# Optimization experiments

Measured on AMD Instinct MI355X. Metric: run time of the kernel, lower is better.

The kernel has to match this reference:

```python
import jax, jax.numpy as jnp
import numpy as np

# Module hyperparameters (from init_kwargs)
K = 1.0                       # init_curvature (registered buffer, non-trainable)
HOPFIELD_DIM = 64
BETA = 1.0 / np.sqrt(float(HOPFIELD_DIM))  # beta=None default -> 1/sqrt(d_h)
EPS = 1e-7

# ---- Lorentz / hyperboloid ops (geoopt conventions, curvature param k>0) ----

def _to_tangent0(x):
    # x: (..., d) Euclidean -> (..., d+1) in T_0 H via [0, x], norm-clipped to 3.5
    zeros = jnp.zeros(x.shape[:-1] + (1,), x.dtype)
    x = jnp.concatenate([zeros, x], axis=-1)
    n = jnp.linalg.norm(x, axis=-1, keepdims=True)
    factor = jnp.minimum(3.5 / (n + 1e-7), 1.0)
    return x * factor

def expmap0(x_euc):
    # (..., d) Euclidean -> (..., d+1) on hyperboloid via Exp_0([0, x])
    u = _to_tangent0(x_euc)
    x = u[..., 1:]
    sqrtk = jnp.sqrt(K)
    xn = jnp.maximum(jnp.linalg.norm(x, axis=-1, keepdims=True), EPS)
    theta = xn / sqrtk
    return jnp.concatenate(
        [sqrtk * jnp.cosh(theta), sqrtk * jnp.sinh(theta) * x / xn], axis=-1)

def logmap0(y):
    # (..., d+1) on hyperboloid -> (..., d) tangent at origin (spatial part)
    sqrtk = jnp.sqrt(K)
    y0 = y[..., :1]
    yr = y[..., 1:]
    yn = jnp.maximum(jnp.linalg.norm(yr, axis=-1, keepdims=True), EPS)
    d = sqrtk * jnp.arccosh(jnp.maximum(y0 / sqrtk, 1.0 + EPS))
    return d * yr / yn

def minkowski_inner(u, v):
    # <u,v>_L = -u0 v0 + sum_i u_i v_i ; returns (...) without last dim
    return -u[..., 0] * v[..., 0] + jnp.sum(u[..., 1:] * v[..., 1:], axis=-1)

# ---- KFCore forward ----

def _kfcore(queries, keys, values, Wq, bq, Wk, bk, Wv, bv):
    sqrtk = jnp.sqrt(K)
    Qe = queries @ Wq.T + bq                     # (B,S,d_h)
    Ke = keys @ Wk.T + bk                        # (B,M,d_h)
    Ve = (values @ Wk.T + bk) @ Wv.T + bv        # (B,M,d_out)
    Q = expmap0(Qe)                              # (B,S,d+1)
    Kh = expmap0(Ke)                             # (B,M,d+1)
    V = expmap0(Ve)                              # (B,M,d+1)

    dp1 = Q.shape[-1]
    sign = jnp.concatenate([-jnp.ones((1,), Q.dtype), jnp.ones((dp1 - 1,), Q.dtype)])

    # Minkowski inner pairwise: (B,S,M)
    sims = jnp.einsum('bsd,bmd->bsm', Q * sign, Kh)
    alpha = jax.nn.softmax(-BETA * sims, axis=-1)          # (B,S,M)

    # Karcher flow: tangent_mean = sum_m alpha * logmap_Q(V_m)
    # logmap_x(y) = dist(x,y) * (y + (<x,y>/k) x) / ||y + (<x,y>/k) x||_L
    ip = jnp.einsum('bsd,bmd->bsm', Q * sign, V)           # <Q_s, V_m>_L
    dist = sqrtk * jnp.arccosh(jnp.maximum(-ip / K, 1.0 + EPS))
    qq = minkowski_inner(Q, Q)[:, :, None]                 # (B,S,1)
    vv = minkowski_inner(V, V)[:, None, :]                 # (B,1,M)
    c = ip / K
    nomin_sq = vv + 2.0 * c * ip + c * c * qq              # ||nomin||_L^2, (B,S,M)
    denom = jnp.sqrt(jnp.maximum(nomin_sq, EPS))
    w = alpha * dist / denom                               # (B,S,M)
    # sum_m w * (V_m + c * Q_s)  -- avoids the (B,S,M,d+1) logmap tensor
    tm = jnp.einsum('bsm,bmd->bsd', w, V) \
         + jnp.sum(w * c, axis=-1, keepdims=True) * Q      # (B,S,d+1)

    # expmap_Q(tm) = cosh(||tm||/sqrtk) Q + sqrtk sinh(||tm||/sqrtk) tm/||tm||
    un = jnp.sqrt(jnp.maximum(minkowski_inner(tm, tm), EPS))[..., None]
    th = un / sqrtk
    z = jnp.cosh(th) * Q + sqrtk * jnp.sinh(th) * tm / un
    return logmap0(z)                                      # (B,S,d_out)


def setup_inputs() -> dict:
    key = jax.random.key(0)
    ks = jax.random.split(key, 9)
    B, S, M = 2, 2048, 4096
    SD, MD, DH, DO = 256, 256, 64, 64
    sq = 1.0 / np.sqrt(SD)
    sm = 1.0 / np.sqrt(MD)
    sh = 1.0 / np.sqrt(DH)
    return {
        'queries': jax.random.normal(ks[0], (B, S, SD), jnp.float32),
        'keys':    jax.random.normal(ks[1], (B, M, MD), jnp.float32),
        'values':  jax.random.normal(ks[2], (B, M, MD), jnp.float32),
        'Wq': jax.random.normal(ks[3], (DH, SD), jnp.float32) * sq,
        'bq': jax.random.normal(ks[4], (DH,), jnp.float32) * sq,
        'Wk': jax.random.normal(ks[5], (DH, MD), jnp.float32) * sm,
        'bk': jax.random.normal(ks[6], (DH,), jnp.float32) * sm,
        'Wv': jax.random.normal(ks[7], (DO, DH), jnp.float32) * sh,
        'bv': jax.random.normal(ks[8], (DO,), jnp.float32) * sh,
    }


def reference(queries, keys, values, Wq, bq, Wk, bk, Wv, bv):
    return _kfcore(queries, keys, values, Wq, bq, Wk, bk, Wv, bv)
```

## Files before the change

kernel.cpp:

```cpp
#include <hip/hip_runtime.h>
#include <math.h>

#define BETA  0.125f
#define SHIFT 30.0f
#define EPSF  1e-7f

typedef __attribute__((ext_vector_type(8))) short short8;
typedef __attribute__((ext_vector_type(4))) short short4v;
typedef __attribute__((ext_vector_type(4))) float f32x4;

__device__ __forceinline__ unsigned short bf16_rne(float x) {
  unsigned int u = __float_as_uint(x);
  return (unsigned short)((u + 0x7fffu + ((u >> 16) & 1u)) >> 16);
}
__device__ __forceinline__ float bf16_tof(unsigned short h) {
  return __uint_as_float(((unsigned int)h) << 16);
}
__device__ __forceinline__ void split2(float x, unsigned short& h, unsigned short& l) {
  unsigned int u = __float_as_uint(x);
  unsigned int hr = (u + 0x7fffu + ((u >> 16) & 1u)) & 0xffff0000u;
  h = (unsigned short)(hr >> 16);
  l = bf16_rne(x - __uint_as_float(hr));
}

#define ZERO_F4 68608

__global__ __launch_bounds__(256) void proj_kernel(
    const float* __restrict__ Xq, const float* __restrict__ Xk,
    const float* __restrict__ Xv,
    const float* __restrict__ Wq, const float* __restrict__ bq,
    const float* __restrict__ Wk, const float* __restrict__ bk,
    const float* __restrict__ Wv, const float* __restrict__ bv,
    float* __restrict__ Q0, float* __restrict__ K0, float* __restrict__ V0,
    unsigned short* __restrict__ Qh, unsigned short* __restrict__ Ql,
    unsigned short* __restrict__ Kh, unsigned short* __restrict__ Kl,
    unsigned short* __restrict__ Vh, unsigned short* __restrict__ Vl,
    unsigned short* __restrict__ Vth, unsigned short* __restrict__ Vtl,
    float* __restrict__ zeroRegion)
{
  __shared__ float Xs[32 * 64];
  __shared__ float Ws[64 * 64];
  __shared__ unsigned int Tr[32 * 65];

  const int bid = blockIdx.x;
  const int tid = threadIdx.x;

  {
    int idx = bid * 256 + tid;
    if (idx < ZERO_F4)
      *(float4*)&zeroRegion[idx * 4] = make_float4(0.f, 0.f, 0.f, 0.f);
  }

  const float *X, *W, *bias;
  float* y0;
  unsigned short *yh, *yl;
  bool dbl;
  int rowBase;
  if (bid < 256)      { X = Xv; W = Wk; bias = bk; y0 = V0; yh = Vh; yl = Vl; rowBase = bid << 5;         dbl = true;  }
  else if (bid < 512) { X = Xk; W = Wk; bias = bk; y0 = K0; yh = Kh; yl = Kl; rowBase = (bid - 256) << 5; dbl = false; }
  else                { X = Xq; W = Wq; bias = bq; y0 = Q0; yh = Qh; yl = Ql; rowBase = (bid - 512) << 5; dbl = false; }

  const int ty = tid >> 4, tx = tid & 15;
  const int ty2 = ty << 1, tx4 = tx << 2;
  const int tyq = ty >> 1;

  float acc[2][4];
#pragma unroll
  for (int j = 0; j < 4; ++j) {
    float bj = bias[tx4 + j];
#pragma unroll
    for (int i = 0; i < 2; ++i) acc[i][j] = bj;
  }

  for (int kc = 0; kc < 4; ++kc) {
#pragma unroll
    for (int q = 0; q < 2; ++q) {
      int f = tid + (q << 8);
      int r = f >> 4, g = f & 15;
      int sw = (r << 6) + ((g ^ (r >> 2)) << 2);
      *(float4*)&Xs[sw] = *(const float4*)&X[(rowBase + r) * 256 + (kc << 6) + (g << 2)];
    }
#pragma unroll
    for (int q = 0; q < 4; ++q) {
      int f = tid + (q << 8);
      int r = f >> 4, g = f & 15;
      int sw = (r << 6) + ((g ^ (r >> 2)) << 2);
      *(float4*)&Ws[sw] = *(const float4*)&W[r * 256 + (kc << 6) + (g << 2)];
    }
    __syncthreads();
#pragma unroll 4
    for (int kk = 0; kk < 64; kk += 4) {
      const int gk = kk >> 2;
      float4 xa[2], wb[4];
#pragma unroll
      for (int i = 0; i < 2; ++i)
        xa[i] = *(const float4*)&Xs[((ty2 + i) << 6) + ((gk ^ tyq) << 2)];
#pragma unroll
      for (int j = 0; j < 4; ++j)
        wb[j] = *(const float4*)&Ws[((tx4 + j) << 6) + ((gk ^ tx) << 2)];
#pragma unroll
      for (int i = 0; i < 2; ++i)
#pragma unroll
        for (int j = 0; j < 4; ++j)
          acc[i][j] += xa[i].x * wb[j].x + xa[i].y * wb[j].y +
                       xa[i].z * wb[j].z + xa[i].w * wb[j].w;
    }
    __syncthreads();
  }

  if (dbl) {
#pragma unroll
    for (int i = 0; i < 2; ++i) {
      float4 v = make_float4(acc[i][0], acc[i][1], acc[i][2], acc[i][3]);
      *(float4*)&Xs[((ty2 + i) << 6) + ((tx ^ tyq) << 2)] = v;
    }
#pragma unroll
    for (int q = 0; q < 4; ++q) {
      int f = tid + (q << 8);
      int r = f >> 4, g = f & 15;
      int sw = (r << 6) + ((g ^ (r >> 2)) << 2);
      *(float4*)&Ws[sw] = *(const float4*)&Wv[(r << 6) + (g << 2)];
    }
#pragma unroll
    for (int j = 0; j < 4; ++j) {
      float bj = bv[tx4 + j];
#pragma unroll
      for (int i = 0; i < 2; ++i) acc[i][j] = bj;
    }
    __syncthreads();
#pragma unroll 4
    for (int kk = 0; kk < 64; kk += 4) {
      const int gk = kk >> 2;
      float4 xa[2], wb[4];
#pragma unroll
      for (int i = 0; i < 2; ++i)
        xa[i] = *(const float4*)&Xs[((ty2 + i) << 6) + ((gk ^ tyq) << 2)];
#pragma unroll
      for (int j = 0; j < 4; ++j)
        wb[j] = *(const float4*)&Ws[((tx4 + j) << 6) + ((gk ^ tx) << 2)];
#pragma unroll
      for (int i = 0; i < 2; ++i)
#pragma unroll
        for (int j = 0; j < 4; ++j)
          acc[i][j] += xa[i].x * wb[j].x + xa[i].y * wb[j].y +
                       xa[i].z * wb[j].z + xa[i].w * wb[j].w;
    }
  }

  float n2p[2];
#pragma unroll
  for (int i = 0; i < 2; ++i)
    n2p[i] = acc[i][0] * acc[i][0] + acc[i][1] * acc[i][1] +
             acc[i][2] * acc[i][2] + acc[i][3] * acc[i][3];
#pragma unroll
  for (int i = 0; i < 2; ++i) {
    n2p[i] += __shfl_xor(n2p[i], 1);
    n2p[i] += __shfl_xor(n2p[i], 2);
    n2p[i] += __shfl_xor(n2p[i], 4);
    n2p[i] += __shfl_xor(n2p[i], 8);
  }
  unsigned short hv[2][4], lv[2][4];
#pragma unroll
  for (int i = 0; i < 2; ++i) {
    float n = sqrtf(n2p[i]);
    float factor = fminf(3.5f / (n + EPSF), 1.0f);
    float xn = fmaxf(n * factor, EPSF);
    float et = __expf(xn);
    float rt = __builtin_amdgcn_rcpf(et);
    float ch = 0.5f * (et + rt);
    float sh = 0.5f * (et - rt);
    float scale = sh * factor * __builtin_amdgcn_rcpf(xn);
    int row = rowBase + ty2 + i;
    if (tx == 0) y0[row] = ch;
#pragma unroll
    for (int j = 0; j < 4; ++j) split2(acc[i][j] * scale, hv[i][j], lv[i][j]);
    unsigned int* ph = (unsigned int*)(yh + row * 64 + tx4);
    ph[0] = (unsigned int)hv[i][0] | ((unsigned int)hv[i][1] << 16);
    ph[1] = (unsigned int)hv[i][2] | ((unsigned int)hv[i][3] << 16);
    unsigned int* pl = (unsigned int*)(yl + row * 64 + tx4);
    pl[0] = (unsigned int)lv[i][0] | ((unsigned int)lv[i][1] << 16);
    pl[1] = (unsigned int)lv[i][2] | ((unsigned int)lv[i][3] << 16);
  }

  if (dbl) {
#pragma unroll
    for (int i = 0; i < 2; ++i)
#pragma unroll
      for (int j = 0; j < 4; ++j)
        Tr[(ty2 + i) * 65 + tx4 + j] = (unsigned int)hv[i][j];
    __syncthreads();
    {
      int d = tid >> 2;
      int seg = (tid & 3) << 3;
      unsigned int o[4];
#pragma unroll
      for (int k = 0; k < 4; ++k)
        o[k] = Tr[(seg + 2 * k) * 65 + d] | (Tr[(seg + 2 * k + 1) * 65 + d] << 16);
      *(uint4*)&Vth[d * 8192 + rowBase + seg] = make_uint4(o[0], o[1], o[2], o[3]);
    }
    __syncthreads();
#pragma unroll
    for (int i = 0; i < 2; ++i)
#pragma unroll
      for (int j = 0; j < 4; ++j)
        Tr[(ty2 + i) * 65 + tx4 + j] = (unsigned int)lv[i][j];
    __syncthreads();
    {
      int d = tid >> 2;
      int seg = (tid & 3) << 3;
      unsigned int o[4];
#pragma unroll
      for (int k = 0; k < 4; ++k)
        o[k] = Tr[(seg + 2 * k) * 65 + d] | (Tr[(seg + 2 * k + 1) * 65 + d] << 16);
      *(uint4*)&Vtl[d * 8192 + rowBase + seg] = make_uint4(o[0], o[1], o[2], o[3]);
    }
  }
}

__global__ void __attribute__((amdgpu_waves_per_eu(2, 2)))
__launch_bounds__(256) attn_kernel(
    const float* __restrict__ Q0g, const unsigned short* __restrict__ Qh,
    const unsigned short* __restrict__ Ql,
    const float* __restrict__ K0g, const unsigned short* __restrict__ Khg,
    const unsigned short* __restrict__ Klg,
    const float* __restrict__ V0g, const unsigned short* __restrict__ Vhg,
    const unsigned short* __restrict__ Vlg,
    const unsigned short* __restrict__ Vthg, const unsigned short* __restrict__ Vtlg,
    float* __restrict__ Tacc, float* __restrict__ T0acc,
    float* __restrict__ Lacc, float* __restrict__ WCacc)
{
  __shared__ unsigned short LB[6 * 4608];

  const int tid = threadIdx.x;
  const int wave = tid >> 6, lane = tid & 63;
  const int lm = lane & 15;
  const int lg = lane >> 4;
  const int bid = blockIdx.x;
  const int slice = bid & 15;
  const int t = bid >> 4;
  const int b = t >> 4;
  const int sT = t & 15;
  const int sBase = b * 2048 + sT * 128 + wave * 32;

  unsigned short* wbase = LB + wave * 2176;

  short8 qf[2][2][2];
#pragma unroll
  for (int si = 0; si < 2; ++si)
#pragma unroll
    for (int ks = 0; ks < 2; ++ks) {
      int idx = (sBase + si * 16 + lm) * 64 + ks * 32 + lg * 8;
      qf[si][ks][0] = *(const short8*)(Qh + idx);
      qf[si][ks][1] = *(const short8*)(Ql + idx);
    }
  float q0r[2][4];
#pragma unroll
  for (int si = 0; si < 2; ++si)
#pragma unroll
    for (int r = 0; r < 4; ++r)
      q0r[si][r] = Q0g[sBase + si * 16 + lg * 4 + r];

  f32x4 accT[2][4];
  float Lp[2][4], WCp[2][4], T0p[2][4];
#pragma unroll
  for (int si = 0; si < 2; ++si)
#pragma unroll
    for (int r = 0; r < 4; ++r) {
      Lp[si][r] = 0.f; WCp[si][r] = 0.f; T0p[si][r] = 0.f;
    }
#pragma unroll
  for (int si = 0; si < 2; ++si)
#pragma unroll
    for (int dj = 0; dj < 4; ++dj) accT[si][dj] = f32x4{0.f, 0.f, 0.f, 0.f};

  const int mSliceBase = b * 4096 + slice * 256;
  const int frow = tid >> 3;
  const int fc8 = (tid & 7) << 3;
  for (int mc = 0; mc < 4; ++mc) {
    const int mCh = mSliceBase + (mc << 6);

#pragma unroll
    for (int q = 0; q < 2; ++q) {
      int row = frow + (q << 5);
      int goff = (mCh + row) * 64 + fc8;
      int loff = row * 72 + fc8;
      *(uint4*)&LB[loff]            = *(const uint4*)&Khg[goff];
      *(uint4*)&LB[4608 + loff]     = *(const uint4*)&Klg[goff];
      *(uint4*)&LB[2 * 4608 + loff] = *(const uint4*)&Vhg[goff];
      *(uint4*)&LB[3 * 4608 + loff] = *(const uint4*)&Vlg[goff];
      int gofft = row * 8192 + mCh + fc8;
      *(uint4*)&LB[4 * 4608 + loff] = *(const uint4*)&Vthg[gofft];
      *(uint4*)&LB[5 * 4608 + loff] = *(const uint4*)&Vtlg[gofft];
    }
    float k0r[4], v0r[4];
#pragma unroll
    for (int mj = 0; mj < 4; ++mj) {
      k0r[mj] = K0g[mCh + mj * 16 + lm];
      v0r[mj] = V0g[mCh + mj * 16 + lm];
    }
    __syncthreads();

    f32x4 sims[2][4], ipv[2][4];
#pragma unroll
    for (int si = 0; si < 2; ++si)
#pragma unroll
      for (int mj = 0; mj < 4; ++mj) {
        sims[si][mj] = f32x4{0.f, 0.f, 0.f, 0.f};
        ipv[si][mj]  = f32x4{0.f, 0.f, 0.f, 0.f};
      }
#pragma unroll
    for (int mj = 0; mj < 4; ++mj) {
#pragma unroll
      for (int ks = 0; ks < 2; ++ks) {
        int off = (mj * 16 + lm) * 72 + ks * 32 + lg * 8;
        short8 kh = *(const short8*)&LB[off];
        short8 kl = *(const short8*)&LB[4608 + off];
        short8 vh = *(const short8*)&LB[2 * 4608 + off];
        short8 vl = *(const short8*)&LB[3 * 4608 + off];
#pragma unroll
        for (int si = 0; si < 2; ++si) {
          sims[si][mj] = __builtin_amdgcn_mfma_f32_16x16x32_bf16(qf[si][ks][0], kh, sims[si][mj], 0, 0, 0);
          sims[si][mj] = __builtin_amdgcn_mfma_f32_16x16x32_bf16(qf[si][ks][0], kl, sims[si][mj], 0, 0, 0);
          sims[si][mj] = __builtin_amdgcn_mfma_f32_16x16x32_bf16(qf[si][ks][1], kh, sims[si][mj], 0, 0, 0);
          ipv[si][mj]  = __builtin_amdgcn_mfma_f32_16x16x32_bf16(qf[si][ks][0], vh, ipv[si][mj], 0, 0, 0);
          ipv[si][mj]  = __builtin_amdgcn_mfma_f32_16x16x32_bf16(qf[si][ks][0], vl, ipv[si][mj], 0, 0, 0);
          ipv[si][mj]  = __builtin_amdgcn_mfma_f32_16x16x32_bf16(qf[si][ks][1], vh, ipv[si][mj], 0, 0, 0);
        }
      }
    }
    __syncthreads();

#pragma unroll
    for (int si = 0; si < 2; ++si)
#pragma unroll
      for (int mj = 0; mj < 4; ++mj)
#pragma unroll
        for (int r = 0; r < 4; ++r) {
          float c  = ipv[si][mj][r]  - q0r[si][r] * v0r[mj];
          float sm = sims[si][mj][r] - q0r[si][r] * k0r[mj];
          float x = -c;
          float s2 = fmaxf(fmaf(x, x, -1.0f), EPSF);
          float rs = __builtin_amdgcn_rsqf(s2);
          float dist = __logf(fmaf(s2, rs, x));
          float e = __expf(fmaf(-BETA, sm, -SHIFT));
          float w = e * dist * rs;
          unsigned short wu = bf16_rne(w);
          float wb = bf16_tof(wu);
          Lp[si][r]  += e;
          WCp[si][r] += wb * c;
          T0p[si][r] += wb * v0r[mj];
          wbase[(si * 16 + lg * 4 + r) * 68 + mj * 16 + lm] = wu;
        }

#pragma unroll
    for (int ks = 0; ks < 2; ++ks) {
      short8 wa[2];
#pragma unroll
      for (int si = 0; si < 2; ++si) {
        const unsigned short* p = wbase + (si * 16 + lm) * 68 + ks * 32 + lg * 8;
        short4v a0 = *(const short4v*)p;
        short4v a1 = *(const short4v*)(p + 4);
        wa[si] = __builtin_shufflevector(a0, a1, 0, 1, 2, 3, 4, 5, 6, 7);
      }
#pragma unroll
      for (int dj = 0; dj < 4; ++dj) {
        int off = (dj * 16 + lm) * 72 + ks * 32 + lg * 8;
        short8 th = *(const short8*)&LB[4 * 4608 + off];
        short8 tl = *(const short8*)&LB[5 * 4608 + off];
#pragma unroll
        for (int si = 0; si < 2; ++si) {
          accT[si][dj] = __builtin_amdgcn_mfma_f32_16x16x32_bf16(wa[si], th, accT[si][dj], 0, 0, 0);
          accT[si][dj] = __builtin_amdgcn_mfma_f32_16x16x32_bf16(wa[si], tl, accT[si][dj], 0, 0, 0);
        }
      }
    }
    __syncthreads();
  }

#pragma unroll
  for (int si = 0; si < 2; ++si)
#pragma unroll
    for (int r = 0; r < 4; ++r)
#pragma unroll
      for (int off = 1; off < 16; off <<= 1) {
        Lp[si][r]  += __shfl_xor(Lp[si][r], off);
        WCp[si][r] += __shfl_xor(WCp[si][r], off);
        T0p[si][r] += __shfl_xor(T0p[si][r], off);
      }

#pragma unroll
  for (int si = 0; si < 2; ++si)
#pragma unroll
    for (int r = 0; r < 4; ++r) {
      int row = sBase + si * 16 + lg * 4 + r;
#pragma unroll
      for (int dj = 0; dj < 4; ++dj)
        unsafeAtomicAdd(&Tacc[row * 64 + dj * 16 + lm], accT[si][dj][r]);
      if (lm == 0) {
        unsafeAtomicAdd(&Lacc[row],  Lp[si][r]);
        unsafeAtomicAdd(&WCacc[row], WCp[si][r]);
        unsafeAtomicAdd(&T0acc[row], T0p[si][r]);
      }
    }
}

__global__ __launch_bounds__(256) void combine_kernel(
    const float* __restrict__ Q0, const unsigned short* __restrict__ Qh,
    const unsigned short* __restrict__ Ql,
    const float* __restrict__ Tacc, const float* __restrict__ T0acc,
    const float* __restrict__ Lacc, const float* __restrict__ WCacc,
    float* __restrict__ out)
{
  int wid = (blockIdx.x << 2) + (threadIdx.x >> 6);
  int lane = threadIdx.x & 63;

  int qi = wid * 64 + lane;
  float Tsum = Tacc[qi];
  float T0 = T0acc[wid];
  float L  = Lacc[wid];
  float WC = WCacc[wid];

  float qd = bf16_tof(Qh[qi]) + bf16_tof(Ql[qi]);
  float q0 = Q0[wid];
  float invL = 1.0f / L;
  float td = Tsum * invL;
  float t0 = T0 * invL;
  float wc = WC * invL;

  double tt = (double)td * (double)td;
#pragma unroll
  for (int off = 1; off < 64; off <<= 1) tt += __shfl_xor(tt, off);
  tt -= (double)t0 * (double)t0;
  double mk = tt + (double)wc * (double)wc;

  float un = (float)sqrt(fmax(mk, 1e-12));
  float eu = __expf(un);
  float ru = 1.0f / eu;
  float ch = 0.5f * (eu + ru);
  float shu = 0.5f * (eu - ru) / un;

  float tmd = td + wc * qd;
  float tm0 = t0 + wc * q0;
  float zd = ch * qd + shu * tmd;
  float z0 = ch * q0 + shu * tm0;

  float p2 = zd * zd;
#pragma unroll
  for (int off = 1; off < 64; off <<= 1) p2 += __shfl_xor(p2, off);
  float yn = fmaxf(sqrtf(p2), EPSF);
  float zc = fmaxf(z0, 1.0f + EPSF);
  float dl = __logf(zc + sqrtf(fmaxf(zc * zc - 1.0f, 0.f)));
  out[qi] = dl * zd / yn;
}

extern "C" void kernel_launch(void* const* d_in, const int* in_sizes, int n_in,
                              void* d_out, int out_size, void* d_ws, size_t ws_size,
                              hipStream_t stream)
{
  const float* queries = (const float*)d_in[0];
  const float* keys    = (const float*)d_in[1];
  const float* values  = (const float*)d_in[2];
  const float* Wq      = (const float*)d_in[3];
  const float* bq      = (const float*)d_in[4];
  const float* Wk      = (const float*)d_in[5];
  const float* bk      = (const float*)d_in[6];
  const float* Wv      = (const float*)d_in[7];
  const float* bv      = (const float*)d_in[8];
  float* out = (float*)d_out;
  float* ws  = (float*)d_ws;

  float* Q0 = ws;
  float* K0 = ws + 4096;
  float* V0 = ws + 12288;
  unsigned short* Qh  = (unsigned short*)(ws + 20480);
  unsigned short* Ql  = (unsigned short*)(ws + 151552);
  unsigned short* Kh  = (unsigned short*)(ws + 282624);
  unsigned short* Kl  = (unsigned short*)(ws + 544768);
  unsigned short* Vh  = (unsigned short*)(ws + 806912);
  unsigned short* Vl  = (unsigned short*)(ws + 1069056);
  unsigned short* Vth = (unsigned short*)(ws + 1331200);
  unsigned short* Vtl = (unsigned short*)(ws + 1593344);
  float* Tacc  = ws + 1855488;
  float* T0acc = ws + 2117632;
  float* Lacc  = ws + 2121728;
  float* WCacc = ws + 2125824;

  proj_kernel<<<640, 256, 0, stream>>>(queries, keys, values, Wq, bq, Wk, bk,
                                       Wv, bv, Q0, K0, V0, Qh, Ql, Kh, Kl,
                                       Vh, Vl, Vth, Vtl, Tacc);
  attn_kernel<<<512, 256, 0, stream>>>(
      Q0, Qh, Ql, K0, Kh, Kl, V0, Vh, Vl, Vth, Vtl,
      Tacc, T0acc, Lacc, WCacc);
  combine_kernel<<<1024, 256, 0, stream>>>(
      Q0, Qh, Ql, Tacc, T0acc, Lacc, WCacc, out);
}
```

Measured before the change: 157.5 us.

## Fuse projection, attention and combine into one persistent kernel with grid barriers

Merges the three kernels into a single 512-block persistent kernel. Blocks 0–127 each take a second projection tile, and software grid barriers built on an atomic counter separate the projection, attention and combine phases. This removes two kernel launches and their gaps. In exchange it adds a memset launch, requires all 512 blocks to be co-resident (enforced via waves_per_eu), and leaves the projection phase load-imbalanced.

```diff
diff --git a/kernel.cpp b/kernel.cpp
--- a/kernel.cpp
+++ b/kernel.cpp
@@ -25,7 +25,20 @@
 
 #define ZERO_F4 68608
 
-__global__ __launch_bounds__(256) void proj_kernel(
+__device__ __forceinline__ void gbar(unsigned int* cnt, unsigned int target) {
+  __syncthreads();
+  if (threadIdx.x == 0) {
+    __threadfence();
+    atomicAdd(cnt, 1u);
+    while (__hip_atomic_load(cnt, __ATOMIC_RELAXED, __HIP_MEMORY_SCOPE_AGENT) < target)
+      __builtin_amdgcn_s_sleep(8);
+  }
+  __syncthreads();
+  __threadfence();
+}
+
+__global__ void __attribute__((amdgpu_waves_per_eu(2, 2)))
+__launch_bounds__(256) fused_kernel(
     const float* __restrict__ Xq, const float* __restrict__ Xk,
     const float* __restrict__ Xv,
     const float* __restrict__ Wq, const float* __restrict__ bq,
@@ -36,421 +49,420 @@
     unsigned short* __restrict__ Kh, unsigned short* __restrict__ Kl,
     unsigned short* __restrict__ Vh, unsigned short* __restrict__ Vl,
     unsigned short* __restrict__ Vth, unsigned short* __restrict__ Vtl,
-    float* __restrict__ zeroRegion)
+    float* __restrict__ Tacc, float* __restrict__ T0acc,
+    float* __restrict__ Lacc, float* __restrict__ WCacc,
+    unsigned int* __restrict__ bar, float* __restrict__ out)
 {
-  __shared__ float Xs[32 * 64];
-  __shared__ float Ws[64 * 64];
-  __shared__ unsigned int Tr[32 * 65];
+  __shared__ unsigned short LB[6 * 4608];
 
   const int bid = blockIdx.x;
   const int tid = threadIdx.x;
 
   {
-    int idx = bid * 256 + tid;
-    if (idx < ZERO_F4)
-      *(float4*)&zeroRegion[idx * 4] = make_float4(0.f, 0.f, 0.f, 0.f);
-  }
-
-  const float *X, *W, *bias;
-  float* y0;
-  unsigned short *yh, *yl;
-  bool dbl;
-  int rowBase;
-  if (bid < 256)      { X = Xv; W = Wk; bias = bk; y0 = V0; yh = Vh; yl = Vl; rowBase = bid << 5;         dbl = true;  }
-  else if (bid < 512) { X = Xk; W = Wk; bias = bk; y0 = K0; yh = Kh; yl = Kl; rowBase = (bid - 256) << 5; dbl = false; }
-  else                { X = Xq; W = Wq; bias = bq; y0 = Q0; yh = Qh; yl = Ql; rowBase = (bid - 512) << 5; dbl = false; }
-
-  const int ty = tid >> 4, tx = tid & 15;
-  const int ty2 = ty << 1, tx4 = tx << 2;
-  const int tyq = ty >> 1;
-
-  float acc[2][4];
-#pragma unroll
-  for (int j = 0; j < 4; ++j) {
-    float bj = bias[tx4 + j];
-#pragma unroll
-    for (int i = 0; i < 2; ++i) acc[i][j] = bj;
-  }
-
-  for (int kc = 0; kc < 4; ++kc) {
-#pragma unroll
-    for (int q = 0; q < 2; ++q) {
-      int f = tid + (q << 8);
-      int r = f >> 4, g = f & 15;
-      int sw = (r << 6) + ((g ^ (r >> 2)) << 2);
-      *(float4*)&Xs[sw] = *(const float4*)&X[(rowBase + r) * 256 + (kc << 6) + (g << 2)];
+    float* Xs = (float*)(void*)LB;
+    float* Ws = (float*)(void*)(LB + 4096);
+    unsigned int* Tr = (unsigned int*)(void*)(LB + 12288);
+
+    {
+      int idx = bid * 256 + tid;
+      if (idx < ZERO_F4)
+        *(float4*)&Tacc[idx * 4] = make_float4(0.f, 0.f, 0.f, 0.f);
     }
-#pragma unroll
-    for (int q = 0; q < 4; ++q) {
-      int f = tid + (q << 8);
-      int r = f >> 4, g = f & 15;
-      int sw = (r << 6) + ((g ^ (r >> 2)) << 2);
-      *(float4*)&Ws[sw] = *(const float4*)&W[r * 256 + (kc << 6) + (g << 2)];
-    }
-    __syncthreads();
+
+    const int ty = tid >> 4, tx = tid & 15;
+    const int ty2 = ty << 1, tx4 = tx << 2;
+    const int tyq = ty >> 1;
+
+    for (int pass = 0; pass < 2; ++pass) {
+      if (pass == 1 && bid >= 128) break;
+      const int t = bid + pass * 512;
+
+      const float *X, *W, *bias;
+      float* y0;
+      unsigned short *yh, *yl;
+      bool dbl;
+      int rowBase;
+      if (t < 256)      { X = Xv; W = Wk; bias = bk; y0 = V0; yh = Vh; yl = Vl; rowBase = t << 5;         dbl = true;  }
+      else if (t < 512) { X = Xk; W = Wk; bias = bk; y0 = K0; yh = Kh; yl = Kl; rowBase = (t - 256) << 5; dbl = false; }
+      else              { X = Xq; W = Wq; bias = bq; y0 = Q0; yh = Qh; yl = Ql; rowBase = (t - 512) << 5; dbl = false; }
+
+      __syncthreads();
+
+      float acc[2][4];
+#pragma unroll
+      for (int j = 0; j < 4; ++j) {
+        float bj = bias[tx4 + j];
+#pragma unroll
+        for (int i = 0; i < 2; ++i) acc[i][j] = bj;
+      }
+
+      for (int kc = 0; kc < 4; ++kc) {
+#pragma unroll
+        for (int q = 0; q < 2; ++q) {
+          int f = tid + (q << 8);
+          int r = f >> 4, g = f & 15;
+          int sw = (r << 6) + ((g ^ (r >> 2)) << 2);
+          *(float4*)&Xs[sw] = *(const float4*)&X[(rowBase + r) * 256 + (kc << 6) + (g << 2)];
+        }
+#pragma unroll
+        for (int q = 0; q < 4; ++q) {
+          int f = tid + (q << 8);
+          int r = f >> 4, g = f & 15;
+          int sw = (r << 6) + ((g ^ (r >> 2)) << 2);
+          *(float4*)&Ws[sw] = *(const float4*)&W[r * 256 + (kc << 6) + (g << 2)];
+        }
+        __syncthreads();
 #pragma unroll 4
-    for (int kk = 0; kk < 64; kk += 4) {
-      const int gk = kk >> 2;
-      float4 xa[2], wb[4];
+        for (int kk = 0; kk < 64; kk += 4) {
+          const int gk = kk >> 2;
+          float4 xa[2], wb[4];
+#pragma unroll
+          for (int i = 0; i < 2; ++i)
+            xa[i] = *(const float4*)&Xs[((ty2 + i) << 6) + ((gk ^ tyq) << 2)];
+#pragma unroll
+          for (int j = 0; j < 4; ++j)
+            wb[j] = *(const float4*)&Ws[((tx4 + j) << 6) + ((gk ^ tx) << 2)];
+#pragma unroll
+          for (int i = 0; i < 2; ++i)
+#pragma unroll
+            for (int j = 0; j < 4; ++j)
+              acc[i][j] += xa[i].x * wb[j].x + xa[i].y * wb[j].y +
+                           xa[i].z * wb[j].z + xa[i].w * wb[j].w;
+        }
+        __syncthreads();
+      }
+
+      if (dbl) {
+#pragma unroll
+        for (int i = 0; i < 2; ++i) {
+          float4 v = make_float4(acc[i][0], acc[i][1], acc[i][2], acc[i][3]);
+          *(float4*)&Xs[((ty2 + i) << 6) + ((tx ^ tyq) << 2)] = v;
+        }
+#pragma unroll
+        for (int q = 0; q < 4; ++q) {
+          int f = tid + (q << 8);
+          int r = f >> 4, g = f & 15;
+          int sw = (r << 6) + ((g ^ (r >> 2)) << 2);
+          *(float4*)&Ws[sw] = *(const float4*)&Wv[(r << 6) + (g << 2)];
+        }
+#pragma unroll
+        for (int j = 0; j < 4; ++j) {
+          float bj = bv[tx4 + j];
+#pragma unroll
+          for (int i = 0; i < 2; ++i) acc[i][j] = bj;
+        }
+        __syncthreads();
+#pragma unroll 4
+        for (int kk = 0; kk < 64; kk += 4) {
+          const int gk = kk >> 2;
+          float4 xa[2], wb[4];
+#pragma unroll
+          for (int i = 0; i < 2; ++i)
+            xa[i] = *(const float4*)&Xs[((ty2 + i) << 6) + ((gk ^ tyq) << 2)];
+#pragma unroll
+          for (int j = 0; j < 4; ++j)
+            wb[j] = *(const float4*)&Ws[((tx4 + j) << 6) + ((gk ^ tx) << 2)];
+#pragma unroll
+          for (int i = 0; i < 2; ++i)
+#pragma unroll
+            for (int j = 0; j < 4; ++j)
+              acc[i][j] += xa[i].x * wb[j].x + xa[i].y * wb[j].y +
+                           xa[i].z * wb[j].z + xa[i].w * wb[j].w;
+        }
+      }
+
+      float n2p[2];
 #pragma unroll
       for (int i = 0; i < 2; ++i)
-        xa[i] = *(const float4*)&Xs[((ty2 + i) << 6) + ((gk ^ tyq) << 2)];
-#pragma unroll
-      for (int j = 0; j < 4; ++j)
-        wb[j] = *(const float4*)&Ws[((tx4 + j) << 6) + ((gk ^ tx) << 2)];
-#pragma unroll
-      for (int i = 0; i < 2; ++i)
-#pragma unroll
-        for (int j = 0; j < 4; ++j)
-          acc[i][j] += xa[i].x * wb[j].x + xa[i].y * wb[j].y +
-                       xa[i].z * wb[j].z + xa[i].w * wb[j].w;
-    }
-    __syncthreads();
-  }
-
-  if (dbl) {
-#pragma unroll
-    for (int i = 0; i < 2; ++i) {
-      float4 v = make_float4(acc[i][0], acc[i][1], acc[i][2], acc[i][3]);
-      *(float4*)&Xs[((ty2 + i) << 6) + ((tx ^ tyq) << 2)] = v;
-    }
-#pragma unroll
-    for (int q = 0; q < 4; ++q) {
-      int f = tid + (q << 8);
-      int r = f >> 4, g = f & 15;
-      int sw = (r << 6) + ((g ^ (r >> 2)) << 2);
-      *(float4*)&Ws[sw] = *(const float4*)&Wv[(r << 6) + (g << 2)];
-    }
-#pragma unroll
-    for (int j = 0; j < 4; ++j) {
-      float bj = bv[tx4 + j];
-#pragma unroll
-      for (int i = 0; i < 2; ++i) acc[i][j] = bj;
-    }
-    __syncthreads();
-#pragma unroll 4
-    for (int kk = 0; kk < 64; kk += 4) {
-      const int gk = kk >> 2;
-      float4 xa[2], wb[4];
-#pragma unroll
-      for (int i = 0; i < 2; ++i)
-        xa[i] = *(const float4*)&Xs[((ty2 + i) << 6) + ((gk ^ tyq) << 2)];
-#pragma unroll
-      for (int j = 0; j < 4; ++j)
-        wb[j] = *(const float4*)&Ws[((tx4 + j) << 6) + ((gk ^ tx) << 2)];
-#pragma unroll
-      for (int i = 0; i < 2; ++i)
-#pragma unroll
-        for (int j = 0; j < 4; ++j)
-          acc[i][j] += xa[i].x * wb[j].x + xa[i].y * wb[j].y +
-                       xa[i].z * wb[j].z + xa[i].w * wb[j].w;
+        n2p[i] = acc[i][0] * acc[i][0] + acc[i][1] * acc[i][1] +
+                 acc[i][2] * acc[i][2] + acc[i][3] * acc[i][3];
+#pragma unroll
+      for (int i = 0; i < 2; ++i) {
+        n2p[i] += __shfl_xor(n2p[i], 1);
+        n2p[i] += __shfl_xor(n2p[i], 2);
+        n2p[i] += __shfl_xor(n2p[i], 4);
+        n2p[i] += __shfl_xor(n2p[i], 8);
+      }
+      unsigned short hv[2][4], lv[2][4];
+#pragma unroll
+      for (int i = 0; i < 2; ++i) {
+        float n = sqrtf(n2p[i]);
+        float factor = fminf(3.5f / (n + EPSF), 1.0f);
+        float xn = fmaxf(n * factor, EPSF);
+        float et = __expf(xn);
+        float rt = __builtin_amdgcn_rcpf(et);
+        float ch = 0.5f * (et + rt);
+        float sh = 0.5f * (et - rt);
+        float scale = sh * factor * __builtin_amdgcn_rcpf(xn);
+        int row = rowBase + ty2 + i;
+        if (tx == 0) y0[row] = ch;
+#pragma unroll
+        for (int j = 0; j < 4; ++j) split2(acc[i][j] * scale, hv[i][j], lv[i][j]);
+        unsigned int* ph = (unsigned int*)(yh + row * 64 + tx4);
+        ph[0] = (unsigned int)hv[i][0] | ((unsigned int)hv[i][1] << 16);
+        ph[1] = (unsigned int)hv[i][2] | ((unsigned int)hv[i][3] << 16);
+        unsigned int* pl = (unsigned int*)(yl + row * 64 + tx4);
+        pl[0] = (unsigned int)lv[i][0] | ((unsigned int)lv[i][1] << 16);
+        pl[1] = (unsigned int)lv[i][2] | ((unsigned int)lv[i][3] << 16);
+      }
+
+      if (dbl) {
+#pragma unroll
+        for (int i = 0; i < 2; ++i)
+#pragma unroll
+          for (int j = 0; j < 4; ++j)
+            Tr[(ty2 + i) * 65 + tx4 + j] = (unsigned int)hv[i][j];
+        __syncthreads();
+        {
+          int d = tid >> 2;
+          int seg = (tid & 3) << 3;
+          unsigned int o[4];
+#pragma unroll
+          for (int k = 0; k < 4; ++k)
+            o[k] = Tr[(seg + 2 * k) * 65 + d] | (Tr[(seg + 2 * k + 1) * 65 + d] << 16);
+          *(uint4*)&Vth[d * 8192 + rowBase + seg] = make_uint4(o[0], o[1], o[2], o[3]);
+        }
+        __syncthreads();
+#pragma unroll
+        for (int i = 0; i < 2; ++i)
+#pragma unroll
+          for (int j = 0; j < 4; ++j)
+            Tr[(ty2 + i) * 65 + tx4 + j] = (unsigned int)lv[i][j];
+        __syncthreads();
+        {
+          int d = tid >> 2;
+          int seg = (tid & 3) << 3;
+          unsigned int o[4];
+#pragma unroll
+          for (int k = 0; k < 4; ++k)
+            o[k] = Tr[(seg + 2 * k) * 65 + d] | (Tr[(seg + 2 * k + 1) * 65 + d] << 16);
+          *(uint4*)&Vtl[d * 8192 + rowBase + seg] = make_uint4(o[0], o[1], o[2], o[3]);
+        }
+      }
     }
   }
 
-  float n2p[2];
-#pragma unroll
-  for (int i = 0; i < 2; ++i)
-    n2p[i] = acc[i][0] * acc[i][0] + acc[i][1] * acc[i][1] +
-             acc[i][2] * acc[i][2] + acc[i][3] * acc[i][3];
-#pragma unroll
-  for (int i = 0; i < 2; ++i) {
-    n2p[i] += __shfl_xor(n2p[i], 1);
-    n2p[i] += __shfl_xor(n2p[i], 2);
-    n2p[i] += __shfl_xor(n2p[i], 4);
-    n2p[i] += __shfl_xor(n2p[i], 8);
+  gbar(bar, 512u);
+
+  {
+    const int wave = tid >> 6, lane = tid & 63;
+    const int lm = lane & 15;
+    const int lg = lane >> 4;
+    const int slice = bid & 15;
+    const int t = bid >> 4;
+    const int b = t >> 4;
+    const int sT = t & 15;
+    const int sBase = b * 2048 + sT * 128 + wave * 32;
+
+    unsigned short* wbase = LB + wave * 2176;
+
+    short8 qf[2][2][2];
+#pragma unroll
+    for (int si = 0; si < 2; ++si)
+#pragma unroll
+      for (int ks = 0; ks < 2; ++ks) {
+        int idx = (sBase + si * 16 + lm) * 64 + ks * 32 + lg * 8;
+        qf[si][ks][0] = *(const short8*)(Qh + idx);
+        qf[si][ks][1] = *(const short8*)(Ql + idx);
+      }
+    float q0r[2][4];
+#pragma unroll
+    for (int si = 0; si < 2; ++si)
+#pragma unroll
+      for (int r = 0; r < 4; ++r)
+        q0r[si][r] = Q0[sBase + si * 16 + lg * 4 + r];
+
+    f32x4 accT[2][4];
+    float Lp[2][4], WCp[2][4], T0p[2][4];
+#pragma unroll
+    for (int si = 0; si < 2; ++si)
+#pragma unroll
+      for (int r = 0; r < 4; ++r) {
+        Lp[si][r] = 0.f; WCp[si][r] = 0.f; T0p[si][r] = 0.f;
+      }
+#pragma unroll
+    for (int si = 0; si < 2; ++si)
+#pragma unroll
+      for (int dj = 0; dj < 4; ++dj) accT[si][dj] = f32x4{0.f, 0.f, 0.f, 0.f};
+
+    const int mSliceBase = b * 4096 + slice * 256;
+    const int frow = tid >> 3;
+    const int fc8 = (tid & 7) << 3;
+    for (int mc = 0; mc < 4; ++mc) {
+      const int mCh = mSliceBase + (mc << 6);
+
+#pragma unroll
+      for (int q = 0; q < 2; ++q) {
+        int row = frow + (q << 5);
+        int goff = (mCh + row) * 64 + fc8;
+        int loff = row * 72 + fc8;
+        *(uint4*)&LB[loff]            = *(const uint4*)&Kh[goff];
+        *(uint4*)&LB[4608 + loff]     = *(const uint4*)&Kl[goff];
+        *(uint4*)&LB[2 * 4608 + loff] = *(const uint4*)&Vh[goff];
+        *(uint4*)&LB[3 * 4608 + loff] = *(const uint4*)&Vl[goff];
+        int gofft = row * 8192 + mCh + fc8;
+        *(uint4*)&LB[4 * 4608 + loff] = *(const uint4*)&Vth[gofft];
+        *(uint4*)&LB[5 * 4608 + loff] = *(const uint4*)&Vtl[gofft];
+      }
+      float k0r[4], v0r[4];
+#pragma unroll
+      for (int mj = 0; mj < 4; ++mj) {
+        k0r[mj] = K0[mCh + mj * 16 + lm];
+        v0r[mj] = V0[mCh + mj * 16 + lm];
+      }
+      __syncthreads();
+
+      f32x4 sims[2][4], ipv[2][4];
+#pragma unroll
+      for (int si = 0; si < 2; ++si)
+#pragma unroll
+        for (int mj = 0; mj < 4; ++mj) {
+          sims[si][mj] = f32x4{0.f, 0.f, 0.f, 0.f};
+          ipv[si][mj]  = f32x4{0.f, 0.f, 0.f, 0.f};
+        }
+#pragma unroll
+      for (int mj = 0; mj < 4; ++mj) {
+#pragma unroll
+        for (int ks = 0; ks < 2; ++ks) {
+          int off = (mj * 16 + lm) * 72 + ks * 32 + lg * 8;
+          short8 kh = *(const short8*)&LB[off];
+          short8 kl = *(const short8*)&LB[4608 + off];
+          short8 vh = *(const short8*)&LB[2 * 4608 + off];
+          short8 vl = *(const short8*)&LB[3 * 4608 + off];
+#pragma unroll
+          for (int si = 0; si < 2; ++si) {
+            sims[si][mj] = __builtin_amdgcn_mfma_f32_16x16x32_bf16(qf[si][ks][0], kh, sims[si][mj], 0, 0, 0);
+            sims[si][mj] = __builtin_amdgcn_mfma_f32_16x16x32_bf16(qf[si][ks][0], kl, sims[si][mj], 0, 0, 0);
+            sims[si][mj] = __builtin_amdgcn_mfma_f32_16x16x32_bf16(qf[si][ks][1], kh, sims[si][mj], 0, 0, 0);
+            ipv[si][mj]  = __builtin_amdgcn_mfma_f32_16x16x32_bf16(qf[si][ks][0], vh, ipv[si][mj], 0, 0, 0);
+            ipv[si][mj]  = __builtin_amdgcn_mfma_f32_16x16x32_bf16(qf[si][ks][0], vl, ipv[si][mj], 0, 0, 0);
+            ipv[si][mj]  = __builtin_amdgcn_mfma_f32_16x16x32_bf16(qf[si][ks][1], vh, ipv[si][mj], 0, 0, 0);
+          }
+        }
+      }
+      __syncthreads();
+
+#pragma unroll
+      for (int si = 0; si < 2; ++si)
+#pragma unroll
+        for (int mj = 0; mj < 4; ++mj)
+#pragma unroll
+          for (int r = 0; r < 4; ++r) {
+            float c  = ipv[si][mj][r]  - q0r[si][r] * v0r[mj];
+            float sm = sims[si][mj][r] - q0r[si][r] * k0r[mj];
+            float x = -c;
+            float s2 = fmaxf(fmaf(x, x, -1.0f), EPSF);
+            float rs = __builtin_amdgcn_rsqf(s2);
+            float dist = __logf(fmaf(s2, rs, x));
+            float e = __expf(fmaf(-BETA, sm, -SHIFT));
+            float w = e * dist * rs;
+            unsigned short wu = bf16_rne(w);
+            float wb = bf16_tof(wu);
+            Lp[si][r]  += e;
+            WCp[si][r] += wb * c;
+            T0p[si][r] += wb * v0r[mj];
+            wbase[(si * 16 + lg * 4 + r) * 68 + mj * 16 + lm] = wu;
+          }
+
+#pragma unroll
+      for (int ks = 0; ks < 2; ++ks) {
+        short8 wa[2];
+#pragma unroll
+        for (int si = 0; si < 2; ++si) {
+          const unsigned short* p = wbase + (si * 16 + lm) * 68 + ks * 32 + lg * 8;
+          short4v a0 = *(const short4v*)p;
+          short4v a1 = *(const short4v*)(p + 4);
+          wa[si] = __builtin_shufflevector(a0, a1, 0, 1, 2, 3, 4, 5, 6, 7);
+        }
+#pragma unroll
+        for (int dj = 0; dj < 4; ++dj) {
+          int off = (dj * 16 + lm) * 72 + ks * 32 + lg * 8;
+          short8 th = *(const short8*)&LB[4 * 4608 + off];
+          short8 tl = *(const short8*)&LB[5 * 4608 + off];
+#pragma unroll
+          for (int si = 0; si < 2; ++si) {
+            accT[si][dj] = __builtin_amdgcn_mfma_f32_16x16x32_bf16(wa[si], th, accT[si][dj], 0, 0, 0);
+            accT[si][dj] = __builtin_amdgcn_mfma_f32_16x16x32_bf16(wa[si], tl, accT[si][dj], 0, 0, 0);
+          }
+        }
+      }
+      __syncthreads();
+    }
+
+#pragma unroll
+    for (int si = 0; si < 2; ++si)
+#pragma unroll
+      for (int r = 0; r < 4; ++r)
+#pragma unroll
+        for (int off = 1; off < 16; off <<= 1) {
+          Lp[si][r]  += __shfl_xor(Lp[si][r], off);
+          WCp[si][r] += __shfl_xor(WCp[si][r], off);
+          T0p[si][r] += __shfl_xor(T0p[si][r], off);
+        }
+
+#pragma unroll
+    for (int si = 0; si < 2; ++si)
+#pragma unroll
+      for (int r = 0; r < 4; ++r) {
+        int row = sBase + si * 16 + lg * 4 + r;
+#pragma unroll
+        for (int dj = 0; dj < 4; ++dj)
+          unsafeAtomicAdd(&Tacc[row * 64 + dj * 16 + lm], accT[si][dj][r]);
+        if (lm == 0) {
+          unsafeAtomicAdd(&Lacc[row],  Lp[si][r]);
+          unsafeAtomicAdd(&WCacc[row], WCp[si][r]);
+          unsafeAtomicAdd(&T0acc[row], T0p[si][r]);
+        }
+      }
   }
-  unsigned short hv[2][4], lv[2][4];
-#pragma unroll
-  for (int i = 0; i < 2; ++i) {
-    float n = sqrtf(n2p[i]);
-    float factor = fminf(3.5f / (n + EPSF), 1.0f);
-    float xn = fmaxf(n * factor, EPSF);
-    float et = __expf(xn);
-    float rt = __builtin_amdgcn_rcpf(et);
-    float ch = 0.5f * (et + rt);
-    float sh = 0.5f * (et - rt);
-    float scale = sh * factor * __builtin_amdgcn_rcpf(xn);
-    int row = rowBase + ty2 + i;
-    if (tx == 0) y0[row] = ch;
-#pragma unroll
-    for (int j = 0; j < 4; ++j) split2(acc[i][j] * scale, hv[i][j], lv[i][j]);
-    unsigned int* ph = (unsigned int*)(yh + row * 64 + tx4);
-    ph[0] = (unsigned int)hv[i][0] | ((unsigned int)hv[i][1] << 16);
-    ph[1] = (unsigned int)hv[i][2] | ((unsigned int)hv[i][3] << 16);
-    unsigned int* pl = (unsigned int*)(yl + row * 64 + tx4);
-    pl[0] = (unsigned int)lv[i][0] | ((unsigned int)lv[i][1] << 16);
-    pl[1] = (unsigned int)lv[i][2] | ((unsigned int)lv[i][3] << 16);
-  }
-
-  if (dbl) {
-#pragma unroll
-    for (int i = 0; i < 2; ++i)
-#pragma unroll
-      for (int j = 0; j < 4; ++j)
-        Tr[(ty2 + i) * 65 + tx4 + j] = (unsigned int)hv[i][j];
-    __syncthreads();
-    {
-      int d = tid >> 2;
-      int seg = (tid & 3) << 3;
-      unsigned int o[4];
-#pragma unroll
-      for (int k = 0; k < 4; ++k)
-        o[k] = Tr[(seg + 2 * k) * 65 + d] | (Tr[(seg + 2 * k + 1) * 65 + d] << 16);
-      *(uint4*)&Vth[d * 8192 + rowBase + seg] = make_uint4(o[0], o[1], o[2], o[3]);
-    }
-    __syncthreads();
-#pragma unroll
-    for (int i = 0; i < 2; ++i)
-#pragma unroll
-      for (int j = 0; j < 4; ++j)
-        Tr[(ty2 + i) * 65 + tx4 + j] = (unsigned int)lv[i][j];
-    __syncthreads();
-    {
-      int d = tid >> 2;
-      int seg = (tid & 3) << 3;
-      unsigned int o[4];
-#pragma unroll
-      for (int k = 0; k < 4; ++k)
-        o[k] = Tr[(seg + 2 * k) * 65 + d] | (Tr[(seg + 2 * k + 1) * 65 + d] << 16);
-      *(uint4*)&Vtl[d * 8192 + rowBase + seg] = make_uint4(o[0], o[1], o[2], o[3]);
+
+  gbar(bar + 1, 512u);
+
+  {
+    const int wave = tid >> 6, lane = tid & 63;
+    const int wid0 = bid * 4 + wave;
+#pragma unroll
+    for (int half = 0; half < 2; ++half) {
+      int wid = wid0 + half * 2048;
+      int qi = wid * 64 + lane;
+      float Tsum = Tacc[qi];
+      float T0 = T0acc[wid];
+      float L  = Lacc[wid];
+      float WC = WCacc[wid];
+
+      float qd = bf16_tof(Qh[qi]) + bf16_tof(Ql[qi]);
+      float q0 = Q0[wid];
+      float invL = 1.0f / L;
+      float td = Tsum * invL;
+      float t0 = T0 * invL;
+      float wc = WC * invL;
+
+      double tt = (double)td * (double)td;
+#pragma unroll
+      for (int off = 1; off < 64; off <<= 1) tt += __shfl_xor(tt, off);
+      tt -= (double)t0 * (double)t0;
+      double mk = tt + (double)wc * (double)wc;
+
+      float un = (float)sqrt(fmax(mk, 1e-12));
+      float eu = __expf(un);
+      float ru = 1.0f / eu;
+      float ch = 0.5f * (eu + ru);
+      float shu = 0.5f * (eu - ru) / un;
+
+      float tmd = td + wc * qd;
+      float tm0 = t0 + wc * q0;
+      float zd = ch * qd + shu * tmd;
+      float z0 = ch * q0 + shu * tm0;
+
+      float p2 = zd * zd;
+#pragma unroll
+      for (int off = 1; off < 64; off <<= 1) p2 += __shfl_xor(p2, off);
+      float yn = fmaxf(sqrtf(p2), EPSF);
+      float zc = fmaxf(z0, 1.0f + EPSF);
+      float dl = __logf(zc + sqrtf(fmaxf(zc * zc - 1.0f, 0.f)));
+      out[qi] = dl * zd / yn;
     }
   }
-}
-
-__global__ void __attribute__((amdgpu_waves_per_eu(2, 2)))
-__launch_bounds__(256) attn_kernel(
-    const float* __restrict__ Q0g, const unsigned short* __restrict__ Qh,
-    const unsigned short* __restrict__ Ql,
-    const float* __restrict__ K0g, const unsigned short* __restrict__ Khg,
-    const unsigned short* __restrict__ Klg,
-    const float* __restrict__ V0g, const unsigned short* __restrict__ Vhg,
-    const unsigned short* __restrict__ Vlg,
-    const unsigned short* __restrict__ Vthg, const unsigned short* __restrict__ Vtlg,
-    float* __restrict__ Tacc, float* __restrict__ T0acc,
-    float* __restrict__ Lacc, float* __restrict__ WCacc)
-{
-  __shared__ unsigned short LB[6 * 4608];
-
-  const int tid = threadIdx.x;
-  const int wave = tid >> 6, lane = tid & 63;
-  const int lm = lane & 15;
-  const int lg = lane >> 4;
-  const int bid = blockIdx.x;
-  const int slice = bid & 15;
-  const int t = bid >> 4;
-  const int b = t >> 4;
-  const int sT = t & 15;
-  const int sBase = b * 2048 + sT * 128 + wave * 32;
-
-  unsigned short* wbase = LB + wave * 2176;
-
-  short8 qf[2][2][2];
-#pragma unroll
-  for (int si = 0; si < 2; ++si)
-#pragma unroll
-    for (int ks = 0; ks < 2; ++ks) {
-      int idx = (sBase + si * 16 + lm) * 64 + ks * 32 + lg * 8;
-      qf[si][ks][0] = *(const short8*)(Qh + idx);
-      qf[si][ks][1] = *(const short8*)(Ql + idx);
-    }
-  float q0r[2][4];
-#pragma unroll
-  for (int si = 0; si < 2; ++si)
-#pragma unroll
-    for (int r = 0; r < 4; ++r)
-      q0r[si][r] = Q0g[sBase + si * 16 + lg * 4 + r];
-
-  f32x4 accT[2][4];
-  float Lp[2][4], WCp[2][4], T0p[2][4];
-#pragma unroll
-  for (int si = 0; si < 2; ++si)
-#pragma unroll
-    for (int r = 0; r < 4; ++r) {
-      Lp[si][r] = 0.f; WCp[si][r] = 0.f; T0p[si][r] = 0.f;
-    }
-#pragma unroll
-  for (int si = 0; si < 2; ++si)
-#pragma unroll
-    for (int dj = 0; dj < 4; ++dj) accT[si][dj] = f32x4{0.f, 0.f, 0.f, 0.f};
-
-  const int mSliceBase = b * 4096 + slice * 256;
-  const int frow = tid >> 3;
-  const int fc8 = (tid & 7) << 3;
-  for (int mc = 0; mc < 4; ++mc) {
-    const int mCh = mSliceBase + (mc << 6);
-
-#pragma unroll
-    for (int q = 0; q < 2; ++q) {
-      int row = frow + (q << 5);
-      int goff = (mCh + row) * 64 + fc8;
-      int loff = row * 72 + fc8;
-      *(uint4*)&LB[loff]            = *(const uint4*)&Khg[goff];
-      *(uint4*)&LB[4608 + loff]     = *(const uint4*)&Klg[goff];
-      *(uint4*)&LB[2 * 4608 + loff] = *(const uint4*)&Vhg[goff];
-      *(uint4*)&LB[3 * 4608 + loff] = *(const uint4*)&Vlg[goff];
-      int gofft = row * 8192 + mCh + fc8;
-      *(uint4*)&LB[4 * 4608 + loff] = *(const uint4*)&Vthg[gofft];
-      *(uint4*)&LB[5 * 4608 + loff] = *(const uint4*)&Vtlg[gofft];
-    }
-    float k0r[4], v0r[4];
-#pragma unroll
-    for (int mj = 0; mj < 4; ++mj) {
-      k0r[mj] = K0g[mCh + mj * 16 + lm];
-      v0r[mj] = V0g[mCh + mj * 16 + lm];
-    }
-    __syncthreads();
-
-    f32x4 sims[2][4], ipv[2][4];
-#pragma unroll
-    for (int si = 0; si < 2; ++si)
-#pragma unroll
-      for (int mj = 0; mj < 4; ++mj) {
-        sims[si][mj] = f32x4{0.f, 0.f, 0.f, 0.f};
-        ipv[si][mj]  = f32x4{0.f, 0.f, 0.f, 0.f};
-      }
-#pragma unroll
-    for (int mj = 0; mj < 4; ++mj) {
-#pragma unroll
-      for (int ks = 0; ks < 2; ++ks) {
-        int off = (mj * 16 + lm) * 72 + ks * 32 + lg * 8;
-        short8 kh = *(const short8*)&LB[off];
-        short8 kl = *(const short8*)&LB[4608 + off];
-        short8 vh = *(const short8*)&LB[2 * 4608 + off];
-        short8 vl = *(const short8*)&LB[3 * 4608 + off];
-#pragma unroll
-        for (int si = 0; si < 2; ++si) {
-          sims[si][mj] = __builtin_amdgcn_mfma_f32_16x16x32_bf16(qf[si][ks][0], kh, sims[si][mj], 0, 0, 0);
-          sims[si][mj] = __builtin_amdgcn_mfma_f32_16x16x32_bf16(qf[si][ks][0], kl, sims[si][mj], 0, 0, 0);
-          sims[si][mj] = __builtin_amdgcn_mfma_f32_16x16x32_bf16(qf[si][ks][1], kh, sims[si][mj], 0, 0, 0);
-          ipv[si][mj]  = __builtin_amdgcn_mfma_f32_16x16x32_bf16(qf[si][ks][0], vh, ipv[si][mj], 0, 0, 0);
-          ipv[si][mj]  = __builtin_amdgcn_mfma_f32_16x16x32_bf16(qf[si][ks][0], vl, ipv[si][mj], 0, 0, 0);
-          ipv[si][mj]  = __builtin_amdgcn_mfma_f32_16x16x32_bf16(qf[si][ks][1], vh, ipv[si][mj], 0, 0, 0);
-        }
-      }
-    }
-    __syncthreads();
-
-#pragma unroll
-    for (int si = 0; si < 2; ++si)
-#pragma unroll
-      for (int mj = 0; mj < 4; ++mj)
-#pragma unroll
-        for (int r = 0; r < 4; ++r) {
-          float c  = ipv[si][mj][r]  - q0r[si][r] * v0r[mj];
-          float sm = sims[si][mj][r] - q0r[si][r] * k0r[mj];
-          float x = -c;
-          float s2 = fmaxf(fmaf(x, x, -1.0f), EPSF);
-          float rs = __builtin_amdgcn_rsqf(s2);
-          float dist = __logf(fmaf(s2, rs, x));
-          float e = __expf(fmaf(-BETA, sm, -SHIFT));
-          float w = e * dist * rs;
-          unsigned short wu = bf16_rne(w);
-          float wb = bf16_tof(wu);
-          Lp[si][r]  += e;
-          WCp[si][r] += wb * c;
-          T0p[si][r] += wb * v0r[mj];
-          wbase[(si * 16 + lg * 4 + r) * 68 + mj * 16 + lm] = wu;
-        }
-
-#pragma unroll
-    for (int ks = 0; ks < 2; ++ks) {
-      short8 wa[2];
-#pragma unroll
-      for (int si = 0; si < 2; ++si) {
-        const unsigned short* p = wbase + (si * 16 + lm) * 68 + ks * 32 + lg * 8;
-        short4v a0 = *(const short4v*)p;
-        short4v a1 = *(const short4v*)(p + 4);
-        wa[si] = __builtin_shufflevector(a0, a1, 0, 1, 2, 3, 4, 5, 6, 7);
-      }
-#pragma unroll
-      for (int dj = 0; dj < 4; ++dj) {
-        int off = (dj * 16 + lm) * 72 + ks * 32 + lg * 8;
-        short8 th = *(const short8*)&LB[4 * 4608 + off];
-        short8 tl = *(const short8*)&LB[5 * 4608 + off];
-#pragma unroll
-        for (int si = 0; si < 2; ++si) {
-          accT[si][dj] = __builtin_amdgcn_mfma_f32_16x16x32_bf16(wa[si], th, accT[si][dj], 0, 0, 0);
-          accT[si][dj] = __builtin_amdgcn_mfma_f32_16x16x32_bf16(wa[si], tl, accT[si][dj], 0, 0, 0);
-        }
-      }
-    }
-    __syncthreads();
-  }
-
-#pragma unroll
-  for (int si = 0; si < 2; ++si)
-#pragma unroll
-    for (int r = 0; r < 4; ++r)
-#pragma unroll
-      for (int off = 1; off < 16; off <<= 1) {
-        Lp[si][r]  += __shfl_xor(Lp[si][r], off);
-        WCp[si][r] += __shfl_xor(WCp[si][r], off);
-        T0p[si][r] += __shfl_xor(T0p[si][r], off);
-      }
-
-#pragma unroll
-  for (int si = 0; si < 2; ++si)
-#pragma unroll
-    for (int r = 0; r < 4; ++r) {
-      int row = sBase + si * 16 + lg * 4 + r;
-#pragma unroll
-      for (int dj = 0; dj < 4; ++dj)
-        unsafeAtomicAdd(&Tacc[row * 64 + dj * 16 + lm], accT[si][dj][r]);
-      if (lm == 0) {
-        unsafeAtomicAdd(&Lacc[row],  Lp[si][r]);
-        unsafeAtomicAdd(&WCacc[row], WCp[si][r]);
-        unsafeAtomicAdd(&T0acc[row], T0p[si][r]);
-      }
-    }
-}
-
-__global__ __launch_bounds__(256) void combine_kernel(
-    const float* __restrict__ Q0, const unsigned short* __restrict__ Qh,
-    const unsigned short* __restrict__ Ql,
-    const float* __restrict__ Tacc, const float* __restrict__ T0acc,
-    const float* __restrict__ Lacc, const float* __restrict__ WCacc,
-    float* __restrict__ out)
-{
-  int wid = (blockIdx.x << 2) + (threadIdx.x >> 6);
-  int lane = threadIdx.x & 63;
-
-  int qi = wid * 64 + lane;
-  float Tsum = Tacc[qi];
-  float T0 = T0acc[wid];
-  float L  = Lacc[wid];
-  float WC = WCacc[wid];
-
-  float qd = bf16_tof(Qh[qi]) + bf16_tof(Ql[qi]);
-  float q0 = Q0[wid];
-  float invL = 1.0f / L;
-  float td = Tsum * invL;
-  float t0 = T0 * invL;
-  float wc = WC * invL;
-
-  double tt = (double)td * (double)td;
-#pragma unroll
-  for (int off = 1; off < 64; off <<= 1) tt += __shfl_xor(tt, off);
-  tt -= (double)t0 * (double)t0;
-  double mk = tt + (double)wc * (double)wc;
-
-  float un = (float)sqrt(fmax(mk, 1e-12));
-  float eu = __expf(un);
-  float ru = 1.0f / eu;
-  float ch = 0.5f * (eu + ru);
-  float shu = 0.5f * (eu - ru) / un;
-
-  float tmd = td + wc * qd;
-  float tm0 = t0 + wc * q0;
-  float zd = ch * qd + shu * tmd;
-  float z0 = ch * q0 + shu * tm0;
-
-  float p2 = zd * zd;
-#pragma unroll
-  for (int off = 1; off < 64; off <<= 1) p2 += __shfl_xor(p2, off);
-  float yn = fmaxf(sqrtf(p2), EPSF);
-  float zc = fmaxf(z0, 1.0f + EPSF);
-  float dl = __logf(zc + sqrtf(fmaxf(zc * zc - 1.0f, 0.f)));
-  out[qi] = dl * zd / yn;
 }
 
 extern "C" void kernel_launch(void* const* d_in, const int* in_sizes, int n_in,
@@ -484,13 +496,11 @@
   float* T0acc = ws + 2117632;
   float* Lacc  = ws + 2121728;
   float* WCacc = ws + 2125824;
-
-  proj_kernel<<<640, 256, 0, stream>>>(queries, keys, values, Wq, bq, Wk, bk,
-                                       Wv, bv, Q0, K0, V0, Qh, Ql, Kh, Kl,
-                                       Vh, Vl, Vth, Vtl, Tacc);
-  attn_kernel<<<512, 256, 0, stream>>>(
-      Q0, Qh, Ql, K0, Kh, Kl, V0, Vh, Vl, Vth, Vtl,
-      Tacc, T0acc, Lacc, WCacc);
-  combine_kernel<<<1024, 256, 0, stream>>>(
-      Q0, Qh, Ql, Tacc, T0acc, Lacc, WCacc, out);
+  unsigned int* bar = (unsigned int*)(ws + 2129920);
+
+  hipMemsetAsync(bar, 0, 2 * sizeof(unsigned int), stream);
+  fused_kernel<<<512, 256, 0, stream>>>(
+      queries, keys, values, Wq, bq, Wk, bk, Wv, bv,
+      Q0, K0, V0, Qh, Ql, Kh, Kl, Vh, Vl, Vth, Vtl,
+      Tacc, T0acc, Lacc, WCacc, bar, out);
 }
```

After: 286.3 us. 1.82x slower.
